# Kernel optimization log

Hardware: AMD Instinct MI355X
Metric: run time of the kernel (lower is better)

The kernel has to match this reference:

```python
import jax, jax.numpy as jnp
import numpy as np

N, E, F_IN, H, C, G, NC = 50000, 800000, 128, 4, 64, 512, 10
NEG_SLOPE = 0.2


def setup_inputs() -> dict:
    key = jax.random.key(0)
    ks = jax.random.split(key, 16)
    s = lambda fan: 1.0 / np.sqrt(fan)
    inp = {
        'x': jax.random.normal(ks[0], (N, F_IN), jnp.float32),
        'edge_index': jax.random.randint(ks[1], (2, E), 0, N, jnp.int64),
        'batch': jnp.sort(jax.random.randint(ks[2], (N,), 0, G, jnp.int64)),
        # conv1: F_IN -> H*C, concat
        'W1': jax.random.normal(ks[3], (F_IN, H * C), jnp.float32) * s(F_IN),
        'a_src1': jax.random.normal(ks[4], (H, C), jnp.float32) * s(C),
        'a_dst1': jax.random.normal(ks[5], (H, C), jnp.float32) * s(C),
        'b1': jnp.zeros((H * C,), jnp.float32),
        # conv2: H*C -> H*C, concat
        'W2': jax.random.normal(ks[6], (H * C, H * C), jnp.float32) * s(H * C),
        'a_src2': jax.random.normal(ks[7], (H, C), jnp.float32) * s(C),
        'a_dst2': jax.random.normal(ks[8], (H, C), jnp.float32) * s(C),
        'b2': jnp.zeros((H * C,), jnp.float32),
        # conv3: H*C -> C, concat=False (mean over heads)
        'W3': jax.random.normal(ks[9], (H * C, H * C), jnp.float32) * s(H * C),
        'a_src3': jax.random.normal(ks[10], (H, C), jnp.float32) * s(C),
        'a_dst3': jax.random.normal(ks[11], (H, C), jnp.float32) * s(C),
        'b3': jnp.zeros((C,), jnp.float32),
        # final linear: C -> NC
        'Wl': jax.random.normal(ks[12], (C, NC), jnp.float32) * s(C),
        'bl': jnp.zeros((NC,), jnp.float32),
    }
    return inp


def _gat_conv(x, src, dst, W, a_src, a_dst, b, concat):
    n = x.shape[0]
    h = (x @ W).reshape(n, H, C)                       # [N,H,C]
    al_src = jnp.sum(h * a_src, axis=-1)               # [N,H]
    al_dst = jnp.sum(h * a_dst, axis=-1)               # [N,H]
    e = al_src[src] + al_dst[dst]                      # [E',H] per-edge logits
    e = jax.nn.leaky_relu(e, NEG_SLOPE)
    # segment softmax over incoming edges of each dst node
    m = jax.ops.segment_max(e, dst, num_segments=n)
    ex = jnp.exp(e - m[dst])
    z = jax.ops.segment_sum(ex, dst, num_segments=n)
    alpha = ex / (z[dst] + 1e-16)                      # [E',H]
    msg = h[src] * alpha[:, :, None]                   # [E',H,C]
    out = jax.ops.segment_sum(msg, dst, num_segments=n)  # [N,H,C]
    out = out.reshape(n, H * C) if concat else out.mean(axis=1)
    return out + b


def reference(x, edge_index, batch, W1, a_src1, a_dst1, b1, W2, a_src2, a_dst2, b2,
              W3, a_src3, a_dst3, b3, Wl, bl):
    n = x.shape[0]
    loops = jnp.arange(n, dtype=edge_index.dtype)
    src = jnp.concatenate([edge_index[0], loops])      # add self-loops (PyG default)
    dst = jnp.concatenate([edge_index[1], loops])
    h = jax.nn.relu(_gat_conv(x, src, dst, W1, a_src1, a_dst1, b1, True))
    h = jax.nn.relu(_gat_conv(h, src, dst, W2, a_src2, a_dst2, b2, True))
    h = jax.nn.relu(_gat_conv(h, src, dst, W3, a_src3, a_dst3, b3, False))
    # global mean pool over graphs
    sums = jax.ops.segment_sum(h, batch, num_segments=G)          # [G,C]
    cnts = jax.ops.segment_sum(jnp.ones((n,), h.dtype), batch, num_segments=G)
    pooled = sums / jnp.maximum(cnts, 1.0)[:, None]
    # dropout is identity in eval mode
    return pooled @ Wl + bl                                       # [G,NC]
```

## Files before the change

### kernel.cpp

```cpp
#include <hip/hip_runtime.h>

#define N_NODES 50000
#define E_EDGES 800000
#define E_TOT   (E_EDGES + N_NODES)
#define F_INDIM 128
#define NHEAD   4
#define CDIM    64
#define HC      256
#define NGRAPH  512
#define NCLS    10
#define NEG_SLOPE 0.2f
#define AGG_BLOCKS 2048
#define XCHUNKS (N_NODES * F_INDIM / 8)

typedef __attribute__((ext_vector_type(8))) _Float16 f16x8;
typedef __attribute__((ext_vector_type(8))) unsigned short ushort8;
typedef __attribute__((ext_vector_type(4))) float f32x4;

__device__ inline float leakyf(float x) { return x > 0.f ? x : NEG_SLOPE * x; }
__device__ inline unsigned short f2h(float x) {
  _Float16 h = (_Float16)x;
  return __builtin_bit_cast(unsigned short, h);
}
__device__ inline float h2f(unsigned short u) {
  return (float)__builtin_bit_cast(_Float16, u);
}

#define GLL16(gp, lp) \
  __builtin_amdgcn_global_load_lds((const __attribute__((address_space(1))) void*)(gp), \
                                   (__attribute__((address_space(3))) void*)(lp), 16, 0, 0)

__global__ __launch_bounds__(256) void k_init_deg(int* __restrict__ deg) {
  int i = blockIdx.x * 256 + threadIdx.x;
  if (i < N_NODES) deg[i] = 1;
}

__global__ __launch_bounds__(256) void k_hist(const int* __restrict__ ei, int* __restrict__ deg) {
  int e = blockIdx.x * 256 + threadIdx.x;
  if (e < E_EDGES) atomicAdd(&deg[ei[E_EDGES + e]], 1);
}

__global__ __launch_bounds__(256) void k_scan1(const int* __restrict__ deg, int* __restrict__ incl,
                                               int* __restrict__ blksum) {
  __shared__ int s[256];
  int tid = threadIdx.x;
  int i = blockIdx.x * 256 + tid;
  int v = (i < N_NODES) ? deg[i] : 0;
  s[tid] = v;
  __syncthreads();
  for (int d = 1; d < 256; d <<= 1) {
    int t = (tid >= d) ? s[tid - d] : 0;
    __syncthreads();
    s[tid] += t;
    __syncthreads();
  }
  if (i < N_NODES) incl[i] = s[tid];
  if (tid == 255) blksum[blockIdx.x] = s[255];
}

__global__ __launch_bounds__(256) void k_scan2(int* __restrict__ blksum, int nblk) {
  __shared__ int s[256];
  int tid = threadIdx.x;
  int v = (tid < nblk) ? blksum[tid] : 0;
  s[tid] = v;
  __syncthreads();
  for (int d = 1; d < 256; d <<= 1) {
    int t = (tid >= d) ? s[tid - d] : 0;
    __syncthreads();
    s[tid] += t;
    __syncthreads();
  }
  if (tid < nblk) blksum[tid] = s[tid] - v;
}

__global__ __launch_bounds__(256) void k_scan3(const int* __restrict__ deg, int* __restrict__ off,
                                               const int* __restrict__ blksum, int* __restrict__ cursor) {
  int i = blockIdx.x * 256 + threadIdx.x;
  if (i < N_NODES) {
    int excl = off[i] - deg[i] + blksum[blockIdx.x];
    off[i] = excl;
    cursor[i] = excl;
  }
  if (i == 0) off[N_NODES] = E_TOT;
}

__global__ __launch_bounds__(256) void k_fill(const int* __restrict__ ei, int* __restrict__ cursor,
                                              int* __restrict__ csr_src) {
  int idx = blockIdx.x * 256 + threadIdx.x;
  if (idx >= E_TOT) return;
  int s, d;
  if (idx < E_EDGES) { s = ei[idx]; d = ei[E_EDGES + idx]; }
  else               { s = idx - E_EDGES; d = s; }
  int pos = atomicAdd(&cursor[d], 1);
  csr_src[pos] = s;
}

__global__ __launch_bounds__(256) void k_cvt_all(const float* __restrict__ x,
                                                 const float* __restrict__ W1,
                                                 const float* __restrict__ W2,
                                                 const float* __restrict__ W3,
                                                 unsigned short* __restrict__ xh,
                                                 unsigned short* __restrict__ Wt1,
                                                 unsigned short* __restrict__ Wt2,
                                                 unsigned short* __restrict__ Wt3) {
  int i = blockIdx.x * 256 + threadIdx.x;
  if (i < XCHUNKS) {
    float4 v0 = *(const float4*)&x[(size_t)i * 8];
    float4 v1 = *(const float4*)&x[(size_t)i * 8 + 4];
    ushort8 o;
    o[0] = f2h(v0.x); o[1] = f2h(v0.y); o[2] = f2h(v0.z); o[3] = f2h(v0.w);
    o[4] = f2h(v1.x); o[5] = f2h(v1.y); o[6] = f2h(v1.z); o[7] = f2h(v1.w);
    *(ushort8*)&xh[(size_t)i * 8] = o;
    return;
  }
  int j = i - XCHUNKS;
  if (j < F_INDIM * HC) {
    int k = j >> 8, n = j & 255;
    Wt1[n * F_INDIM + k] = f2h(W1[j]);
    return;
  }
  j -= F_INDIM * HC;
  if (j < HC * HC) {
    int k = j >> 8, n = j & 255;
    Wt2[n * HC + k] = f2h(W2[j]);
    return;
  }
  j -= HC * HC;
  if (j < HC * HC) {
    int k = j >> 8, n = j & 255;
    Wt3[n * HC + k] = f2h(W3[j]);
  }
}

template<int K>
__global__ __launch_bounds__(256) void k_gemm_f16(const unsigned short* __restrict__ A,
                                                  const unsigned short* __restrict__ Bt,
                                                  unsigned short* __restrict__ C,
                                                  const float* __restrict__ a_src,
                                                  const float* __restrict__ a_dst,
                                                  float* __restrict__ al_s,
                                                  float* __restrict__ al_d) {
  __shared__ unsigned short As[128 * 64];
  __shared__ unsigned short Bs[128 * 64];
  int tid = threadIdx.x;
  int w = tid >> 6, l = tid & 63;
  int wm = w >> 1, wn = w & 1;
  int m0 = blockIdx.x * 128, n0 = blockIdx.y * 128;
  int fl = l & 15, qq = l >> 4;
  int w32 = w * 32;
  int l3 = l >> 3;
  int csw = (l & 7) ^ (l3 & 7);
  f32x4 acc[4][4] = {};

  for (int k0 = 0; k0 < K; k0 += 64) {
#pragma unroll
    for (int j = 0; j < 4; ++j) {
      int r = w32 + j * 8 + l3;
      GLL16(&A[(size_t)(m0 + r) * K + k0 + csw * 8], &As[(w32 + j * 8) * 64]);
      GLL16(&Bt[(size_t)(n0 + r) * K + k0 + csw * 8], &Bs[(w32 + j * 8) * 64]);
    }
    __syncthreads();
#pragma unroll
    for (int kk = 0; kk < 2; ++kk) {
      f16x8 af[4], bf[4];
      int sl = ((kk * 4 + qq) ^ (fl & 7)) * 8;
#pragma unroll
      for (int f = 0; f < 4; ++f) {
        af[f] = *(const f16x8*)&As[(wm * 64 + f * 16 + fl) * 64 + sl];
        bf[f] = *(const f16x8*)&Bs[(wn * 64 + f * 16 + fl) * 64 + sl];
      }
#pragma unroll
      for (int f = 0; f < 4; ++f)
#pragma unroll
        for (int g = 0; g < 4; ++g)
          acc[f][g] = __builtin_amdgcn_mfma_f32_16x16x32_f16(af[f], bf[g], acc[f][g], 0, 0, 0);
    }
    if (k0 + 64 < K) __syncthreads();
  }

  int cr = qq * 4;
#pragma unroll
  for (int f = 0; f < 4; ++f) {
    int mrow = m0 + wm * 64 + f * 16 + cr;
#pragma unroll
    for (int r = 0; r < 4; ++r) {
      if (mrow + r < N_NODES) {
#pragma unroll
        for (int g = 0; g < 4; ++g)
          C[(size_t)(mrow + r) * HC + n0 + wn * 64 + g * 16 + fl] = f2h(acc[f][g][r]);
      }
    }
  }
  int head = blockIdx.y * 2 + wn;
  float as_r[4], ad_r[4];
#pragma unroll
  for (int g = 0; g < 4; ++g) {
    as_r[g] = a_src[head * 64 + g * 16 + fl];
    ad_r[g] = a_dst[head * 64 + g * 16 + fl];
  }
#pragma unroll
  for (int f = 0; f < 4; ++f) {
#pragma unroll
    for (int r = 0; r < 4; ++r) {
      float ps = 0.f, pd = 0.f;
#pragma unroll
      for (int g = 0; g < 4; ++g) {
        ps = fmaf(as_r[g], acc[f][g][r], ps);
        pd = fmaf(ad_r[g], acc[f][g][r], pd);
      }
#pragma unroll
      for (int o = 1; o < 16; o <<= 1) { ps += __shfl_xor(ps, o); pd += __shfl_xor(pd, o); }
      if (fl == 0) {
        int row = m0 + wm * 64 + f * 16 + cr + r;
        if (row < N_NODES) {
          al_s[row * 4 + head] = ps;
          al_d[row * 4 + head] = pd;
        }
      }
    }
  }
}

template<bool CONCAT>
__global__ __launch_bounds__(256) void k_aggregate(
    const unsigned short* __restrict__ h, const int* __restrict__ off, const int* __restrict__ csr_src,
    const float* __restrict__ al_s, const float* __restrict__ al_d,
    const float* __restrict__ bias, unsigned short* __restrict__ out_h, float* __restrict__ out_f) {
  __shared__ float s_p[4][64][4];
  __shared__ int   s_src[4][64];
  int tid = threadIdx.x;
  int wv = tid >> 6;
  int lane = tid & 63;
  int half_id = lane >> 5;
  int c8 = lane & 31;
  int cg8 = c8 << 3;
  int head = c8 >> 3;

  const int NW = AGG_BLOCKS * 4;
  for (int d = blockIdx.x * 4 + wv; d < N_NODES; d += NW) {
    int lo  = off[d];
    int deg = off[d + 1] - lo;

    float4 adv = *(const float4*)&al_d[(size_t)d * 4];

    float z0 = 0.f, z1 = 0.f, z2 = 0.f, z3 = 0.f;
    for (int e = lane; e < deg; e += 64) {
      int s = csr_src[lo + e];
      float4 asv = *(const float4*)&al_s[(size_t)s * 4];
      float p0 = __expf(leakyf(asv.x + adv.x));
      float p1 = __expf(leakyf(asv.y + adv.y));
      float p2 = __expf(leakyf(asv.z + adv.z));
      float p3 = __expf(leakyf(asv.w + adv.w));
      if (e < 64) {
        s_p[wv][e][0] = p0; s_p[wv][e][1] = p1;
        s_p[wv][e][2] = p2; s_p[wv][e][3] = p3;
        s_src[wv][e] = s;
      }
      z0 += p0; z1 += p1; z2 += p2; z3 += p3;
    }
#pragma unroll
    for (int o = 1; o < 64; o <<= 1) {
      z0 += __shfl_xor(z0, o); z1 += __shfl_xor(z1, o);
      z2 += __shfl_xor(z2, o); z3 += __shfl_xor(z3, o);
    }
    float zih = 1.f / ((head == 0 ? z0 : (head == 1 ? z1 : (head == 2 ? z2 : z3))) + 1e-16f);

    int dcap = min(deg, 64);
    float acc[8] = {};
    int e = half_id;
    for (; e + 14 < dcap; e += 16) {
      int sv[8]; float pv[8]; ushort8 hv[8];
#pragma unroll
      for (int q = 0; q < 8; ++q) {
        int ee = e + q * 2;
        sv[q] = s_src[wv][ee];
        pv[q] = s_p[wv][ee][head];
      }
#pragma unroll
      for (int q = 0; q < 8; ++q) hv[q] = *(const ushort8*)&h[(size_t)sv[q] * HC + cg8];
#pragma unroll
      for (int q = 0; q < 8; ++q)
#pragma unroll
        for (int i = 0; i < 8; ++i) acc[i] = fmaf(pv[q], h2f(hv[q][i]), acc[i]);
    }
    for (; e < dcap; e += 2) {
      int s = s_src[wv][e];
      float p = s_p[wv][e][head];
      ushort8 hv = *(const ushort8*)&h[(size_t)s * HC + cg8];
#pragma unroll
      for (int i = 0; i < 8; ++i) acc[i] = fmaf(p, h2f(hv[i]), acc[i]);
    }
    if (deg > 64) {
      for (int e2 = 64 + half_id; e2 < deg; e2 += 2) {
        int s = csr_src[lo + e2];
        float4 asv = *(const float4*)&al_s[(size_t)s * 4];
        float q0 = __expf(leakyf(asv.x + adv.x));
        float q1 = __expf(leakyf(asv.y + adv.y));
        float q2 = __expf(leakyf(asv.z + adv.z));
        float q3 = __expf(leakyf(asv.w + adv.w));
        float p = head == 0 ? q0 : (head == 1 ? q1 : (head == 2 ? q2 : q3));
        ushort8 hv = *(const ushort8*)&h[(size_t)s * HC + cg8];
#pragma unroll
        for (int i = 0; i < 8; ++i) acc[i] = fmaf(p, h2f(hv[i]), acc[i]);
      }
    }

#pragma unroll
    for (int i = 0; i < 8; ++i) {
      acc[i] *= zih;
      acc[i] += __shfl_xor(acc[i], 32);
    }

    if (CONCAT) {
      if (lane < 32) {
        float4 b0 = *(const float4*)&bias[cg8];
        float4 b1v = *(const float4*)&bias[cg8 + 4];
        ushort8 o;
        o[0] = f2h(fmaxf(acc[0] + b0.x, 0.f));
        o[1] = f2h(fmaxf(acc[1] + b0.y, 0.f));
        o[2] = f2h(fmaxf(acc[2] + b0.z, 0.f));
        o[3] = f2h(fmaxf(acc[3] + b0.w, 0.f));
        o[4] = f2h(fmaxf(acc[4] + b1v.x, 0.f));
        o[5] = f2h(fmaxf(acc[5] + b1v.y, 0.f));
        o[6] = f2h(fmaxf(acc[6] + b1v.z, 0.f));
        o[7] = f2h(fmaxf(acc[7] + b1v.w, 0.f));
        *(ushort8*)&out_h[(size_t)d * HC + cg8] = o;
      }
    } else {
#pragma unroll
      for (int i = 0; i < 8; ++i) {
        acc[i] += __shfl_xor(acc[i], 8);
        acc[i] += __shfl_xor(acc[i], 16);
      }
      if (lane < 8) {
        int c0 = lane << 3;
        float4 bb0 = *(const float4*)&bias[c0];
        float4 bb1 = *(const float4*)&bias[c0 + 4];
        float4 v0, v1;
        v0.x = fmaxf(acc[0] * 0.25f + bb0.x, 0.f);
        v0.y = fmaxf(acc[1] * 0.25f + bb0.y, 0.f);
        v0.z = fmaxf(acc[2] * 0.25f + bb0.z, 0.f);
        v0.w = fmaxf(acc[3] * 0.25f + bb0.w, 0.f);
        v1.x = fmaxf(acc[4] * 0.25f + bb1.x, 0.f);
        v1.y = fmaxf(acc[5] * 0.25f + bb1.y, 0.f);
        v1.z = fmaxf(acc[6] * 0.25f + bb1.z, 0.f);
        v1.w = fmaxf(acc[7] * 0.25f + bb1.w, 0.f);
        *(float4*)&out_f[(size_t)d * CDIM + c0] = v0;
        *(float4*)&out_f[(size_t)d * CDIM + c0 + 4] = v1;
      }
    }
  }
}

__device__ inline int lower_bound_i(const int* __restrict__ a, int n, int key) {
  int lo = 0, hi = n;
  while (lo < hi) { int mid = (lo + hi) >> 1; if (a[mid] < key) lo = mid + 1; else hi = mid; }
  return lo;
}

__global__ __launch_bounds__(256) void k_pool(const float* __restrict__ x, const int* __restrict__ batch,
                                              const float* __restrict__ Wl, const float* __restrict__ bl,
                                              float* __restrict__ out) {
  int g = blockIdx.x, tid = threadIdx.x;
  int lo = lower_bound_i(batch, N_NODES, g);
  int hi = lower_bound_i(batch, N_NODES, g + 1);
  int c = tid & 63, sl = tid >> 6;
  float acc = 0.f;
  for (int n = lo + sl; n < hi; n += 4)
    acc += x[(size_t)n * CDIM + c];
  __shared__ float s[256];
  __shared__ float pooled[64];
  s[tid] = acc;
  __syncthreads();
  if (tid < 64) {
    float cnt = fmaxf((float)(hi - lo), 1.f);
    pooled[tid] = (s[tid] + s[tid + 64] + s[tid + 128] + s[tid + 192]) / cnt;
  }
  __syncthreads();
  if (tid < NCLS) {
    float o = bl[tid];
    for (int cc = 0; cc < CDIM; ++cc)
      o = fmaf(pooled[cc], Wl[cc * NCLS + tid], o);
    out[g * NCLS + tid] = o;
  }
}

extern "C" void kernel_launch(void* const* d_in, const int* in_sizes, int n_in,
                              void* d_out, int out_size, void* d_ws, size_t ws_size,
                              hipStream_t stream) {
  const float* x     = (const float*)d_in[0];
  const int*   ei    = (const int*)d_in[1];
  const int*   batch = (const int*)d_in[2];
  const float* W1  = (const float*)d_in[3];
  const float* as1 = (const float*)d_in[4];
  const float* ad1 = (const float*)d_in[5];
  const float* b1  = (const float*)d_in[6];
  const float* W2  = (const float*)d_in[7];
  const float* as2 = (const float*)d_in[8];
  const float* ad2 = (const float*)d_in[9];
  const float* b2  = (const float*)d_in[10];
  const float* W3  = (const float*)d_in[11];
  const float* as3 = (const float*)d_in[12];
  const float* ad3 = (const float*)d_in[13];
  const float* b3  = (const float*)d_in[14];
  const float* Wl  = (const float*)d_in[15];
  const float* bl  = (const float*)d_in[16];
  float* out = (float*)d_out;

  char* ws = (char*)d_ws;
  size_t o = 0;
  auto alloc = [&](size_t bytes) -> void* {
    void* p = ws + o;
    o += (bytes + 255) & ~(size_t)255;
    return p;
  };
  const size_t NPAD = N_NODES + 128;
  unsigned short* hbuf  = (unsigned short*)alloc((size_t)N_NODES * HC * 2);
  unsigned short* abuf  = (unsigned short*)alloc(NPAD * HC * 2);
  float*          bufC  = (float*)alloc((size_t)N_NODES * CDIM * 4);
  unsigned short* x_h   = (unsigned short*)alloc(NPAD * F_INDIM * 2);
  unsigned short* Wt1   = (unsigned short*)alloc((size_t)HC * F_INDIM * 2);
  unsigned short* Wt2   = (unsigned short*)alloc((size_t)HC * HC * 2);
  unsigned short* Wt3   = (unsigned short*)alloc((size_t)HC * HC * 2);
  float* al_s  = (float*)alloc((size_t)N_NODES * 4 * 4);
  float* al_d  = (float*)alloc((size_t)N_NODES * 4 * 4);
  int*   deg   = (int*)alloc((size_t)N_NODES * 4);
  int*   off   = (int*)alloc((size_t)(N_NODES + 1) * 4);
  int*   cursor= (int*)alloc((size_t)N_NODES * 4);
  int*   blksum= (int*)alloc(1024);
  int*   csr   = (int*)alloc((size_t)E_TOT * 4);

  int nblk = (N_NODES + 255) / 256;
  k_init_deg<<<nblk, 256, 0, stream>>>(deg);
  k_hist<<<(E_EDGES + 255) / 256, 256, 0, stream>>>(ei, deg);
  k_scan1<<<nblk, 256, 0, stream>>>(deg, off, blksum);
  k_scan2<<<1, 256, 0, stream>>>(blksum, nblk);
  k_scan3<<<nblk, 256, 0, stream>>>(deg, off, blksum, cursor);
  k_fill<<<(E_TOT + 255) / 256, 256, 0, stream>>>(ei, cursor, csr);

  int cvt_total = XCHUNKS + F_INDIM * HC + 2 * HC * HC;
  k_cvt_all<<<(cvt_total + 255) / 256, 256, 0, stream>>>(x, W1, W2, W3, x_h, Wt1, Wt2, Wt3);

  dim3 ggrid((N_NODES + 127) / 128, HC / 128);
  k_gemm_f16<F_INDIM><<<ggrid, 256, 0, stream>>>(x_h, Wt1, hbuf, as1, ad1, al_s, al_d);
  k_aggregate<true><<<AGG_BLOCKS, 256, 0, stream>>>(hbuf, off, csr, al_s, al_d, b1, abuf, nullptr);
  k_gemm_f16<HC><<<ggrid, 256, 0, stream>>>(abuf, Wt2, hbuf, as2, ad2, al_s, al_d);
  k_aggregate<true><<<AGG_BLOCKS, 256, 0, stream>>>(hbuf, off, csr, al_s, al_d, b2, abuf, nullptr);
  k_gemm_f16<HC><<<ggrid, 256, 0, stream>>>(abuf, Wt3, hbuf, as3, ad3, al_s, al_d);
  k_aggregate<false><<<AGG_BLOCKS, 256, 0, stream>>>(hbuf, off, csr, al_s, al_d, b3, nullptr, bufC);
  k_pool<<<NGRAPH, 256, 0, stream>>>(bufC, batch, Wl, bl, out);
}
```

Baseline: 402.6 us.

## Split node features into two 128-channel slices to shrink aggregation gather footprint

Feature buffers are stored as two column slices (each N×128 fp16). GEMMs write per-slice outputs and read slice-major A, and aggregation blocks alternate slices, so each gather touches only 256 bytes per row and the working set per pass is halved for cache locality. Four lane groups of 16 each process edges in parallel, with shuffle reduction across them. The final layer writes per-slice partial sums and defers the head mean, bias and relu to the pool kernel. The degree init kernel is replaced by a memset plus +1 in the scan. This adds more blocks per node (two passes over edge softmax work) and extra shuffles.

```diff
diff --git a/kernel.cpp b/kernel.cpp
--- a/kernel.cpp
+++ b/kernel.cpp
@@ -11,6 +11,7 @@
 #define NCLS    10
 #define NEG_SLOPE 0.2f
 #define AGG_BLOCKS 2048
+#define NP (N_NODES + 128)
 #define XCHUNKS (N_NODES * F_INDIM / 8)
 
 typedef __attribute__((ext_vector_type(8))) _Float16 f16x8;
@@ -29,11 +30,6 @@
 #define GLL16(gp, lp) \
   __builtin_amdgcn_global_load_lds((const __attribute__((address_space(1))) void*)(gp), \
                                    (__attribute__((address_space(3))) void*)(lp), 16, 0, 0)
-
-__global__ __launch_bounds__(256) void k_init_deg(int* __restrict__ deg) {
-  int i = blockIdx.x * 256 + threadIdx.x;
-  if (i < N_NODES) deg[i] = 1;
-}
 
 __global__ __launch_bounds__(256) void k_hist(const int* __restrict__ ei, int* __restrict__ deg) {
   int e = blockIdx.x * 256 + threadIdx.x;
@@ -45,7 +41,7 @@
   __shared__ int s[256];
   int tid = threadIdx.x;
   int i = blockIdx.x * 256 + tid;
-  int v = (i < N_NODES) ? deg[i] : 0;
+  int v = (i < N_NODES) ? (deg[i] + 1) : 0;
   s[tid] = v;
   __syncthreads();
   for (int d = 1; d < 256; d <<= 1) {
@@ -77,7 +73,7 @@
                                                const int* __restrict__ blksum, int* __restrict__ cursor) {
   int i = blockIdx.x * 256 + threadIdx.x;
   if (i < N_NODES) {
-    int excl = off[i] - deg[i] + blksum[blockIdx.x];
+    int excl = off[i] - (deg[i] + 1) + blksum[blockIdx.x];
     off[i] = excl;
     cursor[i] = excl;
   }
@@ -132,7 +128,7 @@
   }
 }
 
-template<int K>
+template<int K, bool ASL>
 __global__ __launch_bounds__(256) void k_gemm_f16(const unsigned short* __restrict__ A,
                                                   const unsigned short* __restrict__ Bt,
                                                   unsigned short* __restrict__ C,
@@ -153,11 +149,15 @@
   f32x4 acc[4][4] = {};
 
   for (int k0 = 0; k0 < K; k0 += 64) {
+    int kc = k0 + csw * 8;
 #pragma unroll
     for (int j = 0; j < 4; ++j) {
       int r = w32 + j * 8 + l3;
-      GLL16(&A[(size_t)(m0 + r) * K + k0 + csw * 8], &As[(w32 + j * 8) * 64]);
-      GLL16(&Bt[(size_t)(n0 + r) * K + k0 + csw * 8], &Bs[(w32 + j * 8) * 64]);
+      const unsigned short* ap;
+      if (ASL) ap = &A[(size_t)(kc >> 7) * NP * 128 + (size_t)(m0 + r) * 128 + (kc & 127)];
+      else     ap = &A[(size_t)(m0 + r) * K + kc];
+      GLL16(ap, &As[(w32 + j * 8) * 64]);
+      GLL16(&Bt[(size_t)(n0 + r) * K + kc], &Bs[(w32 + j * 8) * 64]);
     }
     __syncthreads();
 #pragma unroll
@@ -179,6 +179,7 @@
   }
 
   int cr = qq * 4;
+  unsigned short* Cs = C + (size_t)blockIdx.y * NP * 128;
 #pragma unroll
   for (int f = 0; f < 4; ++f) {
     int mrow = m0 + wm * 64 + f * 16 + cr;
@@ -187,7 +188,7 @@
       if (mrow + r < N_NODES) {
 #pragma unroll
         for (int g = 0; g < 4; ++g)
-          C[(size_t)(mrow + r) * HC + n0 + wn * 64 + g * 16 + fl] = f2h(acc[f][g][r]);
+          Cs[(size_t)(mrow + r) * 128 + wn * 64 + g * 16 + fl] = f2h(acc[f][g][r]);
       }
     }
   }
@@ -223,24 +224,32 @@
 
 template<bool CONCAT>
 __global__ __launch_bounds__(256) void k_aggregate(
-    const unsigned short* __restrict__ h, const int* __restrict__ off, const int* __restrict__ csr_src,
+    const unsigned short* __restrict__ h_sl, const int* __restrict__ off,
+    const int* __restrict__ csr_src,
     const float* __restrict__ al_s, const float* __restrict__ al_d,
-    const float* __restrict__ bias, unsigned short* __restrict__ out_h, float* __restrict__ out_f) {
+    const float* __restrict__ bias, unsigned short* __restrict__ out_sl,
+    float* __restrict__ out_pf) {
   __shared__ float s_p[4][64][4];
   __shared__ int   s_src[4][64];
   int tid = threadIdx.x;
   int wv = tid >> 6;
   int lane = tid & 63;
-  int half_id = lane >> 5;
-  int c8 = lane & 31;
-  int cg8 = c8 << 3;
-  int head = c8 >> 3;
-
-  const int NW = AGG_BLOCKS * 4;
-  for (int d = blockIdx.x * 4 + wv; d < N_NODES; d += NW) {
+  int grp = lane >> 4;
+  int cl = lane & 15;
+  int cg = cl << 3;
+  int slice = blockIdx.x & 1;
+  int head = slice * 2 + (cl >> 3);
+  const unsigned short* __restrict__ hs = h_sl + (size_t)slice * NP * 128;
+  float bv[8];
+  if (CONCAT) {
+#pragma unroll
+    for (int i = 0; i < 8; ++i) bv[i] = bias[slice * 128 + cg + i];
+  }
+
+  const int STRIDE = (AGG_BLOCKS / 2) * 4;
+  for (int d = (blockIdx.x >> 1) * 4 + wv; d < N_NODES; d += STRIDE) {
     int lo  = off[d];
     int deg = off[d + 1] - lo;
-
     float4 adv = *(const float4*)&al_d[(size_t)d * 4];
 
     float z0 = 0.f, z1 = 0.f, z2 = 0.f, z3 = 0.f;
@@ -267,31 +276,31 @@
 
     int dcap = min(deg, 64);
     float acc[8] = {};
-    int e = half_id;
-    for (; e + 14 < dcap; e += 16) {
-      int sv[8]; float pv[8]; ushort8 hv[8];
-#pragma unroll
-      for (int q = 0; q < 8; ++q) {
-        int ee = e + q * 2;
+    int e = grp;
+    for (; e + 12 < dcap; e += 16) {
+      int sv[4]; float pv[4]; ushort8 hv[4];
+#pragma unroll
+      for (int q = 0; q < 4; ++q) {
+        int ee = e + q * 4;
         sv[q] = s_src[wv][ee];
         pv[q] = s_p[wv][ee][head];
       }
 #pragma unroll
-      for (int q = 0; q < 8; ++q) hv[q] = *(const ushort8*)&h[(size_t)sv[q] * HC + cg8];
-#pragma unroll
-      for (int q = 0; q < 8; ++q)
+      for (int q = 0; q < 4; ++q) hv[q] = *(const ushort8*)&hs[(size_t)sv[q] * 128 + cg];
+#pragma unroll
+      for (int q = 0; q < 4; ++q)
 #pragma unroll
         for (int i = 0; i < 8; ++i) acc[i] = fmaf(pv[q], h2f(hv[q][i]), acc[i]);
     }
-    for (; e < dcap; e += 2) {
+    for (; e < dcap; e += 4) {
       int s = s_src[wv][e];
       float p = s_p[wv][e][head];
-      ushort8 hv = *(const ushort8*)&h[(size_t)s * HC + cg8];
+      ushort8 hv = *(const ushort8*)&hs[(size_t)s * 128 + cg];
 #pragma unroll
       for (int i = 0; i < 8; ++i) acc[i] = fmaf(p, h2f(hv[i]), acc[i]);
     }
     if (deg > 64) {
-      for (int e2 = 64 + half_id; e2 < deg; e2 += 2) {
+      for (int e2 = 64 + grp; e2 < deg; e2 += 4) {
         int s = csr_src[lo + e2];
         float4 asv = *(const float4*)&al_s[(size_t)s * 4];
         float q0 = __expf(leakyf(asv.x + adv.x));
@@ -299,7 +308,7 @@
         float q2 = __expf(leakyf(asv.z + adv.z));
         float q3 = __expf(leakyf(asv.w + adv.w));
         float p = head == 0 ? q0 : (head == 1 ? q1 : (head == 2 ? q2 : q3));
-        ushort8 hv = *(const ushort8*)&h[(size_t)s * HC + cg8];
+        ushort8 hv = *(const ushort8*)&hs[(size_t)s * 128 + cg];
 #pragma unroll
         for (int i = 0; i < 8; ++i) acc[i] = fmaf(p, h2f(hv[i]), acc[i]);
       }
@@ -307,46 +316,25 @@
 
 #pragma unroll
     for (int i = 0; i < 8; ++i) {
+      acc[i] += __shfl_xor(acc[i], 16);
+      acc[i] += __shfl_xor(acc[i], 32);
       acc[i] *= zih;
-      acc[i] += __shfl_xor(acc[i], 32);
     }
 
     if (CONCAT) {
-      if (lane < 32) {
-        float4 b0 = *(const float4*)&bias[cg8];
-        float4 b1v = *(const float4*)&bias[cg8 + 4];
+      if (lane < 16) {
         ushort8 o;
-        o[0] = f2h(fmaxf(acc[0] + b0.x, 0.f));
-        o[1] = f2h(fmaxf(acc[1] + b0.y, 0.f));
-        o[2] = f2h(fmaxf(acc[2] + b0.z, 0.f));
-        o[3] = f2h(fmaxf(acc[3] + b0.w, 0.f));
-        o[4] = f2h(fmaxf(acc[4] + b1v.x, 0.f));
-        o[5] = f2h(fmaxf(acc[5] + b1v.y, 0.f));
-        o[6] = f2h(fmaxf(acc[6] + b1v.z, 0.f));
-        o[7] = f2h(fmaxf(acc[7] + b1v.w, 0.f));
-        *(ushort8*)&out_h[(size_t)d * HC + cg8] = o;
+#pragma unroll
+        for (int i = 0; i < 8; ++i) o[i] = f2h(fmaxf(acc[i] + bv[i], 0.f));
+        *(ushort8*)&out_sl[(size_t)slice * NP * 128 + (size_t)d * 128 + cg] = o;
       }
     } else {
 #pragma unroll
-      for (int i = 0; i < 8; ++i) {
-        acc[i] += __shfl_xor(acc[i], 8);
-        acc[i] += __shfl_xor(acc[i], 16);
-      }
+      for (int i = 0; i < 8; ++i) acc[i] += __shfl_xor(acc[i], 8);
       if (lane < 8) {
-        int c0 = lane << 3;
-        float4 bb0 = *(const float4*)&bias[c0];
-        float4 bb1 = *(const float4*)&bias[c0 + 4];
-        float4 v0, v1;
-        v0.x = fmaxf(acc[0] * 0.25f + bb0.x, 0.f);
-        v0.y = fmaxf(acc[1] * 0.25f + bb0.y, 0.f);
-        v0.z = fmaxf(acc[2] * 0.25f + bb0.z, 0.f);
-        v0.w = fmaxf(acc[3] * 0.25f + bb0.w, 0.f);
-        v1.x = fmaxf(acc[4] * 0.25f + bb1.x, 0.f);
-        v1.y = fmaxf(acc[5] * 0.25f + bb1.y, 0.f);
-        v1.z = fmaxf(acc[6] * 0.25f + bb1.z, 0.f);
-        v1.w = fmaxf(acc[7] * 0.25f + bb1.w, 0.f);
-        *(float4*)&out_f[(size_t)d * CDIM + c0] = v0;
-        *(float4*)&out_f[(size_t)d * CDIM + c0 + 4] = v1;
+        float* pf = &out_pf[(size_t)slice * N_NODES * CDIM + (size_t)d * CDIM + cg];
+        *(float4*)&pf[0] = make_float4(acc[0], acc[1], acc[2], acc[3]);
+        *(float4*)&pf[4] = make_float4(acc[4], acc[5], acc[6], acc[7]);
       }
     }
   }
@@ -358,16 +346,21 @@
   return lo;
 }
 
-__global__ __launch_bounds__(256) void k_pool(const float* __restrict__ x, const int* __restrict__ batch,
+__global__ __launch_bounds__(256) void k_pool(const float* __restrict__ pf,
+                                              const int* __restrict__ batch,
+                                              const float* __restrict__ b3,
                                               const float* __restrict__ Wl, const float* __restrict__ bl,
                                               float* __restrict__ out) {
   int g = blockIdx.x, tid = threadIdx.x;
   int lo = lower_bound_i(batch, N_NODES, g);
   int hi = lower_bound_i(batch, N_NODES, g + 1);
   int c = tid & 63, sl = tid >> 6;
+  float bc = b3[c];
   float acc = 0.f;
-  for (int n = lo + sl; n < hi; n += 4)
-    acc += x[(size_t)n * CDIM + c];
+  for (int n = lo + sl; n < hi; n += 4) {
+    float v = pf[(size_t)n * CDIM + c] + pf[(size_t)N_NODES * CDIM + (size_t)n * CDIM + c];
+    acc += fmaxf(0.25f * v + bc, 0.f);
+  }
   __shared__ float s[256];
   __shared__ float pooled[64];
   s[tid] = acc;
@@ -414,16 +407,15 @@
     o += (bytes + 255) & ~(size_t)255;
     return p;
   };
-  const size_t NPAD = N_NODES + 128;
-  unsigned short* hbuf  = (unsigned short*)alloc((size_t)N_NODES * HC * 2);
-  unsigned short* abuf  = (unsigned short*)alloc(NPAD * HC * 2);
-  float*          bufC  = (float*)alloc((size_t)N_NODES * CDIM * 4);
-  unsigned short* x_h   = (unsigned short*)alloc(NPAD * F_INDIM * 2);
+  unsigned short* hbuf  = (unsigned short*)alloc((size_t)2 * NP * 128 * 2);
+  unsigned short* abuf  = (unsigned short*)alloc((size_t)2 * NP * 128 * 2);
+  unsigned short* x_h   = (unsigned short*)alloc((size_t)NP * F_INDIM * 2);
   unsigned short* Wt1   = (unsigned short*)alloc((size_t)HC * F_INDIM * 2);
   unsigned short* Wt2   = (unsigned short*)alloc((size_t)HC * HC * 2);
   unsigned short* Wt3   = (unsigned short*)alloc((size_t)HC * HC * 2);
   float* al_s  = (float*)alloc((size_t)N_NODES * 4 * 4);
   float* al_d  = (float*)alloc((size_t)N_NODES * 4 * 4);
+  float* pf    = (float*)alloc((size_t)2 * N_NODES * CDIM * 4);
   int*   deg   = (int*)alloc((size_t)N_NODES * 4);
   int*   off   = (int*)alloc((size_t)(N_NODES + 1) * 4);
   int*   cursor= (int*)alloc((size_t)N_NODES * 4);
@@ -431,7 +423,7 @@
   int*   csr   = (int*)alloc((size_t)E_TOT * 4);
 
   int nblk = (N_NODES + 255) / 256;
-  k_init_deg<<<nblk, 256, 0, stream>>>(deg);
+  hipMemsetAsync(deg, 0, (size_t)N_NODES * 4, stream);
   k_hist<<<(E_EDGES + 255) / 256, 256, 0, stream>>>(ei, deg);
   k_scan1<<<nblk, 256, 0, stream>>>(deg, off, blksum);
   k_scan2<<<1, 256, 0, stream>>>(blksum, nblk);
@@ -442,11 +434,11 @@
   k_cvt_all<<<(cvt_total + 255) / 256, 256, 0, stream>>>(x, W1, W2, W3, x_h, Wt1, Wt2, Wt3);
 
   dim3 ggrid((N_NODES + 127) / 128, HC / 128);
-  k_gemm_f16<F_INDIM><<<ggrid, 256, 0, stream>>>(x_h, Wt1, hbuf, as1, ad1, al_s, al_d);
+  k_gemm_f16<F_INDIM, false><<<ggrid, 256, 0, stream>>>(x_h, Wt1, hbuf, as1, ad1, al_s, al_d);
   k_aggregate<true><<<AGG_BLOCKS, 256, 0, stream>>>(hbuf, off, csr, al_s, al_d, b1, abuf, nullptr);
-  k_gemm_f16<HC><<<ggrid, 256, 0, stream>>>(abuf, Wt2, hbuf, as2, ad2, al_s, al_d);
+  k_gemm_f16<HC, true><<<ggrid, 256, 0, stream>>>(abuf, Wt2, hbuf, as2, ad2, al_s, al_d);
   k_aggregate<true><<<AGG_BLOCKS, 256, 0, stream>>>(hbuf, off, csr, al_s, al_d, b2, abuf, nullptr);
-  k_gemm_f16<HC><<<ggrid, 256, 0, stream>>>(abuf, Wt3, hbuf, as3, ad3, al_s, al_d);
-  k_aggregate<false><<<AGG_BLOCKS, 256, 0, stream>>>(hbuf, off, csr, al_s, al_d, b3, nullptr, bufC);
-  k_pool<<<NGRAPH, 256, 0, stream>>>(bufC, batch, Wl, bl, out);
-}
+  k_gemm_f16<HC, true><<<ggrid, 256, 0, stream>>>(abuf, Wt3, hbuf, as3, ad3, al_s, al_d);
+  k_aggregate<false><<<AGG_BLOCKS, 256, 0, stream>>>(hbuf, off, csr, al_s, al_d, b3, nullptr, pf);
+  k_pool<<<NGRAPH, 256, 0, stream>>>(pf, batch, b3, Wl, bl, out);
+}
```

Measured after the change: 449.2 us. 1.12x slower.
